# Performance work log

Measured on AMD Instinct MI355X. Metric: run time of the kernel, lower is better.

## Reference

```python
import jax, jax.numpy as jnp
import numpy as np


def setup_inputs() -> dict:
    key = jax.random.key(0)
    ks = jax.random.split(key, 5)
    B, Cin, Cout, H, W, L, K = 16, 512, 512, 64, 64, 512, 3
    return {
        "content": jax.random.normal(ks[0], (B, Cin, H, W), jnp.float32),
        "latent": jax.random.normal(ks[1], (B, L), jnp.float32),
        "noise": jax.random.normal(ks[2], (B, 1, H, W), jnp.float32),
        "affine_w": jax.random.normal(ks[3], (Cin, L), jnp.float32),
        "affine_b": jnp.ones((Cin,), jnp.float32),  # ConvLayer fills affine bias with 1
        "conv_w": jax.random.normal(ks[4], (Cout, Cin, K, K), jnp.float32),
        "bias": jnp.zeros((1, Cout, 1, 1), jnp.float32),
        "noise_weight": jnp.asarray(0.1, jnp.float32),  # nonzero so noise path is exercised
    }


def reference(content, latent, noise, affine_w, affine_b, conv_w, bias, noise_weight):
    L = affine_w.shape[1]
    # affine (LinearLayer, lrelu=False): weight scaled by sqrt(1/inChannels), lrMultiplier=1
    style = latent @ (affine_w * np.sqrt(1.0 / L)).T + affine_b  # [B, Cin]
    # modulate: per-sample weights [B, Cout, Cin, k, k]
    w = conv_w[None] * style[:, None, :, None, None]
    # demodulate
    norm = jax.lax.rsqrt(jnp.sum(jnp.square(w), axis=(2, 3, 4), keepdims=True) + 1e-8)
    w = w * norm
    pad = conv_w.shape[-1] // 2
    # groups=batch trick == per-sample conv; vmap over batch
    def conv1(x, wk):  # x: [Cin,H,W], wk: [Cout,Cin,k,k]
        return jax.lax.conv_general_dilated(x[None], wk, (1, 1), [(pad, pad), (pad, pad)])[0]
    out = jax.vmap(conv1)(content, w)  # [B, Cout, H, W]
    out = out + noise_weight * noise
    out = jax.nn.leaky_relu(out + bias, negative_slope=0.2) * np.sqrt(2.0)
    return out
```

## Files before the change

kernel.cpp:

```cpp
#include <hip/hip_runtime.h>
#include <hip/hip_bf16.h>


typedef float f32x4 __attribute__((ext_vector_type(4)));
typedef short bf16x8 __attribute__((ext_vector_type(8)));
typedef int i32x4 __attribute__((ext_vector_type(4)));

#define BB 16
#define CIN 512
#define COUT 512
#define HH 64
#define WW 64
#define LL 512

#define XS2ROWB 81920

#define XS2_OFF 0
#define XS2_SZ (BB * HH * XS2ROWB)
#define WT_OFF (XS2_OFF + XS2_SZ)
#define WT_SZ (9 * COUT * CIN * 2)
#define STYLE_OFF (WT_OFF + WT_SZ)
#define STYLE_SZ (BB * CIN * 4)
#define WSQ_OFF (STYLE_OFF + STYLE_SZ)
#define WSQ_SZ (COUT * CIN * 4)
#define DEM_OFF (WSQ_OFF + WSQ_SZ)
#define DEM_SZ (BB * COUT * 4)
#define ZROW_OFF (DEM_OFF + DEM_SZ)
#define ZROW_SZ XS2ROWB
#define WS_NEEDED (ZROW_OFF + ZROW_SZ)

#define WBUF 36864
#define LDSZ (2 * WBUF)

__device__ __forceinline__ void gld_lds16(const void* g, void* l) {
  __builtin_amdgcn_global_load_lds(
      (const __attribute__((address_space(1))) unsigned int*)g,
      (__attribute__((address_space(3))) unsigned int*)l, 16, 0, 0);
}

__global__ void style_kernel(const float* __restrict__ latent,
                             const float* __restrict__ affine_w,
                             const float* __restrict__ affine_b,
                             float* __restrict__ style) {
  const int idx = blockIdx.x * 256 + threadIdx.x;
  const int b = idx >> 9, ci = idx & 511;
  const float* lp = latent + b * LL;
  const float* wp = affine_w + ci * LL;
  float acc = 0.f;
  for (int l = 0; l < LL; ++l) acc += lp[l] * wp[l];
  style[idx] = acc * 0.044194173824159216f + affine_b[ci];
}

__global__ void wprep_kernel(const float* __restrict__ conv_w,
                             float* __restrict__ wsq,
                             __hip_bfloat16* __restrict__ wt) {
  const int idx = blockIdx.x * 256 + threadIdx.x;
  const int co = idx >> 9, ci = idx & 511;
  const float* wp = conv_w + idx * 9;
  float ss = 0.f;
#pragma unroll
  for (int t = 0; t < 9; ++t) {
    float v = wp[t];
    ss += v * v;
    wt[(t * COUT + co) * CIN + ci] = __float2bfloat16(v);
  }
  wsq[idx] = ss;
}

__global__ void dem_kernel(const float* __restrict__ wsq,
                           const float* __restrict__ style,
                           float* __restrict__ dem) {
  const int idx = blockIdx.x * 256 + threadIdx.x;
  const int b = idx >> 9, co = idx & 511;
  const float* sp = style + b * CIN;
  const float* wp = wsq + co * CIN;
  float acc = 0.f;
  for (int ci = 0; ci < CIN; ++ci) {
    float s = sp[ci];
    acc += wp[ci] * s * s;
  }
  dem[idx] = 1.0f / sqrtf(acc + 1e-8f);
}

__global__ void xsprep_kernel(const float* __restrict__ content,
                              const float* __restrict__ style,
                              __hip_bfloat16* __restrict__ xs2,
                              __hip_bfloat16* __restrict__ zrow) {
  const int tid = threadIdx.x;
  if (blockIdx.x == 1024) {
    for (int off = tid * 16; off < XS2ROWB; off += 256 * 16)
      *(i32x4*)((char*)zrow + off) = (i32x4){0, 0, 0, 0};
    return;
  }
  __shared__ float tile[64][65];
  const int b = blockIdx.x >> 6;
  const int y = blockIdx.x & 63;
  char* row = (char*)xs2 + (size_t)((b << 6) + y) * XS2ROWB;

  for (int k = 0; k < 4; ++k) {
    const int idx = tid + k * 256;
    const int oct = idx >> 4, s = idx & 15;
    const int off = oct * 1280 + (s < 8 ? s * 16 : 1024 + s * 16);
    *(i32x4*)(row + off) = (i32x4){0, 0, 0, 0};
  }

  for (int cb = 0; cb < 8; ++cb) {
    const int ci0 = cb * 64;
    __syncthreads();
    {
      const int x = tid & 63;
      const int c0 = tid >> 6;
#pragma unroll
      for (int p = 0; p < 16; ++p) {
        const int ci = p * 4 + c0;
        tile[ci][x] = content[((b * CIN + ci0 + ci) * HH + y) * WW + x];
      }
    }
    __syncthreads();
    {
      const int x = tid & 63;
      const int o4 = tid >> 6;
      const int px = x + 8;
      const int xoff = ((px >> 4) << 8) + ((px & 15) << 4);
#pragma unroll
      for (int oo = 0; oo < 2; ++oo) {
        const int oct = o4 * 2 + oo;
        bf16x8 v;
#pragma unroll
        for (int j = 0; j < 8; ++j) {
          const float st = style[b * CIN + ci0 + oct * 8 + j];
          v[j] = __bfloat16_as_short(
              __float2bfloat16(tile[oct * 8 + j][x] * st));
        }
        *(bf16x8*)(row + (ci0 / 8 + oct) * 1280 + xoff) = v;
      }
    }
  }
}

__global__ __launch_bounds__(256, 2) void conv_kernel(
    const __hip_bfloat16* __restrict__ xs2,
    const __hip_bfloat16* __restrict__ wt,
    const float* __restrict__ dem,
    const float* __restrict__ noise,
    const float* __restrict__ biasp,
    const float* __restrict__ nwp,
    const __hip_bfloat16* __restrict__ zrow,
    float* __restrict__ out) {
  __shared__ __attribute__((aligned(16))) char lds[2][WBUF];

  const int tid = threadIdx.x;
  const int lane = tid & 63;
  const int wv = tid >> 6;

  const int d = blockIdx.x;
  const int L = (d & 7) * 128 + (d >> 3);
  const int cot = L & 7;
  const int yo = (L >> 3) & 7;
  const int b = L >> 6;
  const int co0 = cot << 6;
  const int y0 = yo << 3;

  const int l15 = lane & 15;
  const int kg = lane >> 4;
  const int xsub = lane >> 2;
  const int slotl = lane & 3;

  int aoff[4];
#pragma unroll
  for (int mf = 0; mf < 4; ++mf) {
    const int co_l = l15 + mf * 16;
    const int fs = (co_l & 3) ^ ((co_l >> 2) & 3);
    aoff[mf] = co_l * 64 + ((kg ^ fs) << 4);
  }

  const char* rp[4];
#pragma unroll
  for (int ir = 0; ir < 4; ++ir) {
    const int yg = y0 + 2 * wv - 1 + ir;
    rp[ir] = (yg >= 0 && yg < 64)
                 ? (const char*)xs2 + (size_t)((b << 6) + yg) * XS2ROWB
                 : (const char*)zrow;
  }
  int voff[4][3];
#pragma unroll
  for (int q = 0; q < 4; ++q)
#pragma unroll
    for (int dx = 0; dx < 3; ++dx) {
      const int p = 7 + q * 16 + l15 + dx;
      voff[q][dx] = kg * 1280 + ((p >> 4) << 8) + ((p & 15) << 4);
    }

  f32x4 acc[4][8];
#pragma unroll
  for (int mf = 0; mf < 4; ++mf)
#pragma unroll
    for (int nf = 0; nf < 8; ++nf) acc[mf][nf] = (f32x4){0.f, 0.f, 0.f, 0.f};

  auto stageW = [&](int cibs, char* wbuf) {
    const int ci0 = cibs * 32;
    for (int i = wv; i < 36; i += 4) {
      const int tap = i >> 2, q = i & 3;
      const int co = q * 16 + xsub;
      const int dcig = slotl ^ ((co & 3) ^ ((co >> 2) & 3));
      const __hip_bfloat16* g =
          wt + ((tap << 9) + co0 + co) * CIN + ci0 + dcig * 8;
      gld_lds16(g, wbuf + tap * 4096 + q * 1024);
    }
  };

  stageW(0, lds[0]);

#pragma unroll 2
  for (int cib = 0; cib < 16; ++cib) {
    __syncthreads();
    if (cib < 15) stageW(cib + 1, lds[(cib + 1) & 1]);
    const char* wb = lds[cib & 1];
    const int cshift = cib * 5120;

#pragma unroll
    for (int dx = 0; dx < 3; ++dx) {
      bf16x8 a[3][4];
#pragma unroll
      for (int dy = 0; dy < 3; ++dy)
#pragma unroll
        for (int mf = 0; mf < 4; ++mf)
          a[dy][mf] = *(const bf16x8*)(wb + (dy * 3 + dx) * 4096 + aoff[mf]);
#pragma unroll
      for (int ir = 0; ir < 4; ++ir) {
        const char* rpc = rp[ir] + cshift;
        bf16x8 bq[4];
#pragma unroll
        for (int q = 0; q < 4; ++q)
          bq[q] = *(const bf16x8*)(rpc + voff[q][dx]);
#pragma unroll
        for (int dy = 0; dy < 3; ++dy) {
          const int r = ir - dy;
          if (r == 0 || r == 1) {
#pragma unroll
            for (int q = 0; q < 4; ++q)
#pragma unroll
              for (int mf = 0; mf < 4; ++mf)
                acc[mf][r * 4 + q] = __builtin_amdgcn_mfma_f32_16x16x32_bf16(
                    a[dy][mf], bq[q], acc[mf][r * 4 + q], 0, 0, 0);
          }
        }
      }
    }
  }

  const float nwv = nwp[0];
#pragma unroll
  for (int r = 0; r < 2; ++r) {
    const int y = y0 + 2 * wv + r;
    float nz[4];
#pragma unroll
    for (int q = 0; q < 4; ++q)
      nz[q] = nwv * noise[(b << 12) + (y << 6) + q * 16 + l15];

#pragma unroll
    for (int mf = 0; mf < 4; ++mf) {
      const int cobase = co0 + mf * 16 + kg * 4;
      const f32x4 dm = *(const f32x4*)(dem + (b << 9) + cobase);
      const f32x4 bs = *(const f32x4*)(biasp + cobase);
#pragma unroll
      for (int r2 = 0; r2 < 4; ++r2) {
        const int co = cobase + r2;
        float* op = out + ((((b << 9) + co) << 12) | (y << 6) | l15);
        const float dmv = dm[r2];
        const float bsv = bs[r2];
#pragma unroll
        for (int q = 0; q < 4; ++q) {
          float v = acc[mf][r * 4 + q][r2] * dmv + nz[q] + bsv;
          v = (v > 0.f ? v : 0.2f * v) * 1.41421356237309515f;
          op[q * 16] = v;
        }
      }
    }
  }
}

extern "C" void kernel_launch(void* const* d_in, const int* in_sizes, int n_in,
                              void* d_out, int out_size, void* d_ws, size_t ws_size,
                              hipStream_t stream) {
  const float* content  = (const float*)d_in[0];
  const float* latent   = (const float*)d_in[1];
  const float* noise    = (const float*)d_in[2];
  const float* affine_w = (const float*)d_in[3];
  const float* affine_b = (const float*)d_in[4];
  const float* conv_w   = (const float*)d_in[5];
  const float* bias     = (const float*)d_in[6];
  const float* nw       = (const float*)d_in[7];
  float* out = (float*)d_out;
  char* ws = (char*)d_ws;

  if (ws_size < (size_t)WS_NEEDED) return;

  __hip_bfloat16* xs2  = (__hip_bfloat16*)(ws + XS2_OFF);
  __hip_bfloat16* wt   = (__hip_bfloat16*)(ws + WT_OFF);
  float* style = (float*)(ws + STYLE_OFF);
  float* wsq   = (float*)(ws + WSQ_OFF);
  float* dem   = (float*)(ws + DEM_OFF);
  __hip_bfloat16* zrow = (__hip_bfloat16*)(ws + ZROW_OFF);

  style_kernel<<<dim3(32), dim3(256), 0, stream>>>(latent, affine_w, affine_b, style);
  wprep_kernel<<<dim3(1024), dim3(256), 0, stream>>>(conv_w, wsq, wt);
  dem_kernel<<<dim3(32), dim3(256), 0, stream>>>(wsq, style, dem);
  xsprep_kernel<<<dim3(1025), dim3(256), 0, stream>>>(content, style, xs2, zrow);
  conv_kernel<<<dim3(1024), dim3(256), 0, stream>>>(xs2, wt, dem, noise, bias, nw, zrow, out);
}
```

Measured before the change: 364.7 us.

## Stage activations in LDS with padded layout and switch to 32x32x16 MFMA

Activations are repacked into a zero-padded per-16-channel layout so the halo rows and columns need no separate zero row. The conv kernel now double-buffers both the activation tile and the weight tile into LDS with global_load_lds, instead of reading activations straight from global memory. It also switches from 16x16x32 to 32x32x16 bf16 MFMA, which cuts the number of operand fetches per FLOP. The cost is more LDS per block, which may limit occupancy, plus new layouts for the weight and activation prep kernels.

Result: faster. 322.3 us (-11.6%).

```diff
diff --git a/kernel.cpp b/kernel.cpp
--- a/kernel.cpp
+++ b/kernel.cpp
@@ -3,6 +3,7 @@
 
 
 typedef float f32x4 __attribute__((ext_vector_type(4)));
+typedef float f32x16 __attribute__((ext_vector_type(16)));
 typedef short bf16x8 __attribute__((ext_vector_type(8)));
 typedef int i32x4 __attribute__((ext_vector_type(4)));
 
@@ -13,24 +14,26 @@
 #define WW 64
 #define LL 512
 
-#define XS2ROWB 81920
-
-#define XS2_OFF 0
-#define XS2_SZ (BB * HH * XS2ROWB)
-#define WT_OFF (XS2_OFF + XS2_SZ)
-#define WT_SZ (9 * COUT * CIN * 2)
-#define STYLE_OFF (WT_OFF + WT_SZ)
+#define X3ROWB 2176
+#define X3C16B (66 * X3ROWB)
+#define X3BB (32 * X3C16B)
+#define XS3_SZ (16 * X3BB)
+
+#define WT3_STEPB 147456
+#define WT3_SZ (32 * WT3_STEPB)
+
+#define XS3_OFF 0
+#define WT3_OFF XS3_SZ
+#define STYLE_OFF (WT3_OFF + WT3_SZ)
 #define STYLE_SZ (BB * CIN * 4)
 #define WSQ_OFF (STYLE_OFF + STYLE_SZ)
 #define WSQ_SZ (COUT * CIN * 4)
 #define DEM_OFF (WSQ_OFF + WSQ_SZ)
 #define DEM_SZ (BB * COUT * 4)
-#define ZROW_OFF (DEM_OFF + DEM_SZ)
-#define ZROW_SZ XS2ROWB
-#define WS_NEEDED (ZROW_OFF + ZROW_SZ)
-
-#define WBUF 36864
-#define LDSZ (2 * WBUF)
+#define WS_NEEDED (DEM_OFF + DEM_SZ)
+
+#define XSTEPB 22528
+#define WSTEPB 18432
 
 __device__ __forceinline__ void gld_lds16(const void* g, void* l) {
   __builtin_amdgcn_global_load_lds(
@@ -53,16 +56,18 @@
 
 __global__ void wprep_kernel(const float* __restrict__ conv_w,
                              float* __restrict__ wsq,
-                             __hip_bfloat16* __restrict__ wt) {
+                             __hip_bfloat16* __restrict__ wt3) {
   const int idx = blockIdx.x * 256 + threadIdx.x;
   const int co = idx >> 9, ci = idx & 511;
   const float* wp = conv_w + idx * 9;
+  const int cib = ci >> 4, h = (ci >> 3) & 1, ci8 = ci & 7;
+  __hip_bfloat16* base = wt3 + (size_t)cib * 73728 + h * 4096 + co * 8 + ci8;
   float ss = 0.f;
 #pragma unroll
   for (int t = 0; t < 9; ++t) {
     float v = wp[t];
     ss += v * v;
-    wt[(t * COUT + co) * CIN + ci] = __float2bfloat16(v);
+    base[t * 8192] = __float2bfloat16(v);
   }
   wsq[idx] = ss;
 }
@@ -84,24 +89,31 @@
 
 __global__ void xsprep_kernel(const float* __restrict__ content,
                               const float* __restrict__ style,
-                              __hip_bfloat16* __restrict__ xs2,
-                              __hip_bfloat16* __restrict__ zrow) {
-  const int tid = threadIdx.x;
-  if (blockIdx.x == 1024) {
-    for (int off = tid * 16; off < XS2ROWB; off += 256 * 16)
-      *(i32x4*)((char*)zrow + off) = (i32x4){0, 0, 0, 0};
-    return;
-  }
+                              char* __restrict__ xs3) {
   __shared__ float tile[64][65];
   const int b = blockIdx.x >> 6;
   const int y = blockIdx.x & 63;
-  char* row = (char*)xs2 + (size_t)((b << 6) + y) * XS2ROWB;
-
-  for (int k = 0; k < 4; ++k) {
-    const int idx = tid + k * 256;
-    const int oct = idx >> 4, s = idx & 15;
-    const int off = oct * 1280 + (s < 8 ? s * 16 : 1024 + s * 16);
-    *(i32x4*)(row + off) = (i32x4){0, 0, 0, 0};
+  const int tid = threadIdx.x;
+  char* bbase = xs3 + (size_t)b * X3BB;
+
+  {
+    const int c16 = tid >> 3, rest = tid & 7;
+    const int h = rest >> 2, pp = rest & 3;
+    const int px = (pp == 0) ? 0 : 64 + pp;
+    *(i32x4*)(bbase + (size_t)c16 * X3C16B + (y + 1) * X3ROWB + h * 1088 +
+              px * 16) = (i32x4){0, 0, 0, 0};
+  }
+  if (y == 0 || y == 63) {
+    const int rowidx = (y == 0) ? 0 : 65;
+#pragma unroll
+    for (int k = 0; k < 17; ++k) {
+      const int u = tid + k * 256;
+      if (u < 4352) {
+        const int c16 = u / 136, w = u - c16 * 136;
+        *(i32x4*)(bbase + (size_t)c16 * X3C16B + rowidx * X3ROWB + w * 16) =
+            (i32x4){0, 0, 0, 0};
+      }
+    }
   }
 
   for (int cb = 0; cb < 8; ++cb) {
@@ -120,11 +132,11 @@
     {
       const int x = tid & 63;
       const int o4 = tid >> 6;
-      const int px = x + 8;
-      const int xoff = ((px >> 4) << 8) + ((px & 15) << 4);
 #pragma unroll
       for (int oo = 0; oo < 2; ++oo) {
         const int oct = o4 * 2 + oo;
+        const int c16 = cb * 4 + (oct >> 1);
+        const int h = oct & 1;
         bf16x8 v;
 #pragma unroll
         for (int j = 0; j < 8; ++j) {
@@ -132,26 +144,29 @@
           v[j] = __bfloat16_as_short(
               __float2bfloat16(tile[oct * 8 + j][x] * st));
         }
-        *(bf16x8*)(row + (ci0 / 8 + oct) * 1280 + xoff) = v;
+        *(bf16x8*)(bbase + (size_t)c16 * X3C16B + (y + 1) * X3ROWB + h * 1088 +
+                   (x + 1) * 16) = v;
       }
     }
   }
 }
 
 __global__ __launch_bounds__(256, 2) void conv_kernel(
-    const __hip_bfloat16* __restrict__ xs2,
-    const __hip_bfloat16* __restrict__ wt,
+    const char* __restrict__ xs3,
+    const char* __restrict__ wt3,
     const float* __restrict__ dem,
     const float* __restrict__ noise,
     const float* __restrict__ biasp,
     const float* __restrict__ nwp,
-    const __hip_bfloat16* __restrict__ zrow,
     float* __restrict__ out) {
-  __shared__ __attribute__((aligned(16))) char lds[2][WBUF];
+  __shared__ __attribute__((aligned(16))) char xlds[2][XSTEPB];
+  __shared__ __attribute__((aligned(16))) char wlds[2][WSTEPB];
 
   const int tid = threadIdx.x;
   const int lane = tid & 63;
   const int wv = tid >> 6;
+  const int l31 = lane & 31;
+  const int hsel = lane >> 5;
 
   const int d = blockIdx.x;
   const int L = (d & 7) * 128 + (d >> 3);
@@ -161,123 +176,132 @@
   const int co0 = cot << 6;
   const int y0 = yo << 3;
 
-  const int l15 = lane & 15;
-  const int kg = lane >> 4;
-  const int xsub = lane >> 2;
-  const int slotl = lane & 3;
-
-  int aoff[4];
-#pragma unroll
-  for (int mf = 0; mf < 4; ++mf) {
-    const int co_l = l15 + mf * 16;
-    const int fs = (co_l & 3) ^ ((co_l >> 2) & 3);
-    aoff[mf] = co_l * 64 + ((kg ^ fs) << 4);
-  }
-
-  const char* rp[4];
-#pragma unroll
-  for (int ir = 0; ir < 4; ++ir) {
-    const int yg = y0 + 2 * wv - 1 + ir;
-    rp[ir] = (yg >= 0 && yg < 64)
-                 ? (const char*)xs2 + (size_t)((b << 6) + yg) * XS2ROWB
-                 : (const char*)zrow;
-  }
-  int voff[4][3];
-#pragma unroll
-  for (int q = 0; q < 4; ++q)
+  const char* xsrc[6];
+#pragma unroll
+  for (int k = 0; k < 6; ++k) {
+    const int c = wv + 4 * k;
+    if (c < 22) {
+      const int beta = c * 1024 + lane * 16;
+      const int row = beta / X3ROWB;
+      const int within = beta - row * X3ROWB;
+      xsrc[k] = xs3 + (size_t)(b * 32) * X3C16B +
+                (size_t)(y0 + row) * X3ROWB + within;
+    } else {
+      xsrc[k] = xs3;
+    }
+  }
+  const char* wsrc[5];
+#pragma unroll
+  for (int k = 0; k < 5; ++k) {
+    const int c = wv + 4 * k;
+    if (c < 18) {
+      const int tap = c >> 1, h = c & 1;
+      wsrc[k] = wt3 + tap * 16384 + h * 8192 + (co0 + lane) * 16;
+    } else {
+      wsrc[k] = wt3;
+    }
+  }
+
+  const int abase0 = hsel * 1024 + l31 * 16;
+  const int bbase0 = hsel * 1088 + l31 * 16;
+  const int xwrow = 2 * wv * X3ROWB;
+
+  f32x16 acc[2][2][2];
+#pragma unroll
+  for (int mf = 0; mf < 2; ++mf)
+#pragma unroll
+    for (int r = 0; r < 2; ++r)
+#pragma unroll
+      for (int q = 0; q < 2; ++q)
+#pragma unroll
+        for (int e = 0; e < 16; ++e) acc[mf][r][q][e] = 0.f;
+
+  auto stage = [&](int t, int bi) {
+    char* xd = xlds[bi];
+    char* wd = wlds[bi];
+    const size_t xadv = (size_t)t * X3C16B;
+    const size_t wadv = (size_t)t * WT3_STEPB;
+#pragma unroll
+    for (int k = 0; k < 6; ++k) {
+      const int c = wv + 4 * k;
+      if (c < 22) gld_lds16(xsrc[k] + xadv, xd + c * 1024);
+    }
+#pragma unroll
+    for (int k = 0; k < 5; ++k) {
+      const int c = wv + 4 * k;
+      if (c < 18) gld_lds16(wsrc[k] + wadv, wd + c * 1024);
+    }
+  };
+
+  stage(0, 0);
+  __syncthreads();
+
+  for (int t = 0; t < 32; ++t) {
+    const int bi = t & 1;
+    if (t < 31) stage(t + 1, bi ^ 1);
+    const char* xb = xlds[bi];
+    const char* wb = wlds[bi];
 #pragma unroll
     for (int dx = 0; dx < 3; ++dx) {
-      const int p = 7 + q * 16 + l15 + dx;
-      voff[q][dx] = kg * 1280 + ((p >> 4) << 8) + ((p & 15) << 4);
-    }
-
-  f32x4 acc[4][8];
-#pragma unroll
-  for (int mf = 0; mf < 4; ++mf)
-#pragma unroll
-    for (int nf = 0; nf < 8; ++nf) acc[mf][nf] = (f32x4){0.f, 0.f, 0.f, 0.f};
-
-  auto stageW = [&](int cibs, char* wbuf) {
-    const int ci0 = cibs * 32;
-    for (int i = wv; i < 36; i += 4) {
-      const int tap = i >> 2, q = i & 3;
-      const int co = q * 16 + xsub;
-      const int dcig = slotl ^ ((co & 3) ^ ((co >> 2) & 3));
-      const __hip_bfloat16* g =
-          wt + ((tap << 9) + co0 + co) * CIN + ci0 + dcig * 8;
-      gld_lds16(g, wbuf + tap * 4096 + q * 1024);
-    }
-  };
-
-  stageW(0, lds[0]);
-
-#pragma unroll 2
-  for (int cib = 0; cib < 16; ++cib) {
-    __syncthreads();
-    if (cib < 15) stageW(cib + 1, lds[(cib + 1) & 1]);
-    const char* wb = lds[cib & 1];
-    const int cshift = cib * 5120;
-
-#pragma unroll
-    for (int dx = 0; dx < 3; ++dx) {
-      bf16x8 a[3][4];
+      bf16x8 a[3][2];
 #pragma unroll
       for (int dy = 0; dy < 3; ++dy)
 #pragma unroll
-        for (int mf = 0; mf < 4; ++mf)
-          a[dy][mf] = *(const bf16x8*)(wb + (dy * 3 + dx) * 4096 + aoff[mf]);
+        for (int mf = 0; mf < 2; ++mf)
+          a[dy][mf] = *(const bf16x8*)(wb + (dy * 3 + dx) * 2048 + abase0 +
+                                       mf * 512);
 #pragma unroll
       for (int ir = 0; ir < 4; ++ir) {
-        const char* rpc = rp[ir] + cshift;
-        bf16x8 bq[4];
-#pragma unroll
-        for (int q = 0; q < 4; ++q)
-          bq[q] = *(const bf16x8*)(rpc + voff[q][dx]);
+        const char* rp = xb + xwrow + ir * X3ROWB;
+        bf16x8 bq[2];
+#pragma unroll
+        for (int q = 0; q < 2; ++q)
+          bq[q] = *(const bf16x8*)(rp + bbase0 + (q * 32 + dx) * 16);
 #pragma unroll
         for (int dy = 0; dy < 3; ++dy) {
           const int r = ir - dy;
           if (r == 0 || r == 1) {
 #pragma unroll
-            for (int q = 0; q < 4; ++q)
-#pragma unroll
-              for (int mf = 0; mf < 4; ++mf)
-                acc[mf][r * 4 + q] = __builtin_amdgcn_mfma_f32_16x16x32_bf16(
-                    a[dy][mf], bq[q], acc[mf][r * 4 + q], 0, 0, 0);
+            for (int q = 0; q < 2; ++q)
+#pragma unroll
+              for (int mf = 0; mf < 2; ++mf)
+                acc[mf][r][q] = __builtin_amdgcn_mfma_f32_32x32x16_bf16(
+                    a[dy][mf], bq[q], acc[mf][r][q], 0, 0, 0);
           }
         }
       }
     }
+    __syncthreads();
   }
 
   const float nwv = nwp[0];
+  float nz[2][2];
 #pragma unroll
   for (int r = 0; r < 2; ++r) {
     const int y = y0 + 2 * wv + r;
-    float nz[4];
-#pragma unroll
-    for (int q = 0; q < 4; ++q)
-      nz[q] = nwv * noise[(b << 12) + (y << 6) + q * 16 + l15];
-
-#pragma unroll
-    for (int mf = 0; mf < 4; ++mf) {
-      const int cobase = co0 + mf * 16 + kg * 4;
-      const f32x4 dm = *(const f32x4*)(dem + (b << 9) + cobase);
-      const f32x4 bs = *(const f32x4*)(biasp + cobase);
-#pragma unroll
-      for (int r2 = 0; r2 < 4; ++r2) {
-        const int co = cobase + r2;
-        float* op = out + ((((b << 9) + co) << 12) | (y << 6) | l15);
-        const float dmv = dm[r2];
-        const float bsv = bs[r2];
-#pragma unroll
-        for (int q = 0; q < 4; ++q) {
-          float v = acc[mf][r * 4 + q][r2] * dmv + nz[q] + bsv;
+#pragma unroll
+    for (int q = 0; q < 2; ++q)
+      nz[r][q] = nwv * noise[(b << 12) + (y << 6) + q * 32 + l31];
+  }
+#pragma unroll
+  for (int mf = 0; mf < 2; ++mf)
+#pragma unroll
+    for (int reg = 0; reg < 16; ++reg) {
+      const int coo = (reg & 3) + 8 * (reg >> 2) + 4 * hsel;
+      const int co = co0 + mf * 32 + coo;
+      const float dv = dem[(b << 9) + co];
+      const float bv = biasp[co];
+#pragma unroll
+      for (int r = 0; r < 2; ++r) {
+        const int y = y0 + 2 * wv + r;
+#pragma unroll
+        for (int q = 0; q < 2; ++q) {
+          float v = acc[mf][r][q][reg] * dv + nz[r][q] + bv;
           v = (v > 0.f ? v : 0.2f * v) * 1.41421356237309515f;
-          op[q * 16] = v;
+          out[(((size_t)(b << 9) + co) << 12) + (y << 6) + q * 32 + l31] = v;
         }
       }
     }
-  }
 }
 
 extern "C" void kernel_launch(void* const* d_in, const int* in_sizes, int n_in,
@@ -296,16 +320,16 @@
 
   if (ws_size < (size_t)WS_NEEDED) return;
 
-  __hip_bfloat16* xs2  = (__hip_bfloat16*)(ws + XS2_OFF);
-  __hip_bfloat16* wt   = (__hip_bfloat16*)(ws + WT_OFF);
+  char* xs3 = ws + XS3_OFF;
+  __hip_bfloat16* wt3 = (__hip_bfloat16*)(ws + WT3_OFF);
   float* style = (float*)(ws + STYLE_OFF);
   float* wsq   = (float*)(ws + WSQ_OFF);
   float* dem   = (float*)(ws + DEM_OFF);
-  __hip_bfloat16* zrow = (__hip_bfloat16*)(ws + ZROW_OFF);
 
   style_kernel<<<dim3(32), dim3(256), 0, stream>>>(latent, affine_w, affine_b, style);
-  wprep_kernel<<<dim3(1024), dim3(256), 0, stream>>>(conv_w, wsq, wt);
+  wprep_kernel<<<dim3(1024), dim3(256), 0, stream>>>(conv_w, wsq, wt3);
   dem_kernel<<<dim3(32), dim3(256), 0, stream>>>(wsq, style, dem);
-  xsprep_kernel<<<dim3(1025), dim3(256), 0, stream>>>(content, style, xs2, zrow);
-  conv_kernel<<<dim3(1024), dim3(256), 0, stream>>>(xs2, wt, dem, noise, bias, nw, zrow, out);
-}
+  xsprep_kernel<<<dim3(1024), dim3(256), 0, stream>>>(content, style, xs3);
+  conv_kernel<<<dim3(1024), dim3(256), 0, stream>>>(
+      xs3, (const char*)(ws + WT3_OFF), dem, noise, bias, nw, out);
+}
```
